# Performance work log

Measured on AMD Instinct MI355X. Metric: run time of the kernel, lower is better.

## Reference

```python
import jax, jax.numpy as jnp
import numpy as np

DIM = 25
N_NODES = 20000
N_EDGES = 320000
NFEAT = 300
NHID = 64
NCLASS = 50


def setup_inputs() -> dict:
    key = jax.random.key(0)
    ks = jax.random.split(key, 8)
    s1 = np.sqrt(6.0 / (NFEAT + NHID))
    s2 = np.sqrt(6.0 / (NHID * DIM + NCLASS))
    return {
        "x": jax.random.normal(ks[0], (N_NODES, NFEAT), dtype=jnp.float32),
        "adj_rows": jax.random.randint(ks[1], (DIM, N_EDGES), 0, N_NODES, dtype=jnp.int32),
        "adj_cols": jax.random.randint(ks[2], (DIM, N_EDGES), 0, N_NODES, dtype=jnp.int32),
        "adj_vals": jax.random.uniform(ks[3], (DIM, N_EDGES), dtype=jnp.float32),
        "W1": jax.random.uniform(ks[4], (DIM, NFEAT, NHID), dtype=jnp.float32, minval=-s1, maxval=s1),
        "b1": jnp.zeros((DIM, NHID), dtype=jnp.float32),
        "W2": jax.random.uniform(ks[5], (DIM, NHID * DIM, NCLASS), dtype=jnp.float32, minval=-s2, maxval=s2),
        "b2": jnp.zeros((DIM, NCLASS), dtype=jnp.float32),
    }


def _spmm(rows, cols, vals, sup, n):
    # sparse [n,n] @ dense [n,f] via gather + segment-sum scatter-add
    return jax.ops.segment_sum(vals[:, None] * sup[cols], rows, num_segments=n)


def reference(x, adj_rows, adj_cols, adj_vals, W1, b1, W2, b2):
    n = x.shape[0]
    spmm = jax.vmap(lambda r, c, v, s: _spmm(r, c, v, s, n))
    # layer 1: per-branch dense mm, spmm, bias, relu  -> [DIM, n, NHID]
    sup1 = jnp.einsum("nf,dfh->dnh", x, W1)
    h1 = jax.nn.relu(spmm(adj_rows, adj_cols, adj_vals, sup1) + b1[:, None, :])
    # permute + reshape: concat branch features per node -> [n, DIM*NHID]
    h1cat = jnp.transpose(h1, (1, 0, 2)).reshape(n, -1)
    # layer 2: per-branch dense mm, spmm, bias, relu -> [DIM, n, NCLASS]
    sup2 = jnp.einsum("nk,dkc->dnc", h1cat, W2)
    h2 = jax.nn.relu(spmm(adj_rows, adj_cols, adj_vals, sup2) + b2[:, None, :])
    # max-pool over branches (POOLING='max')
    return jnp.max(h2, axis=0)
```

## Files before the change

kernel.cpp:

```cpp
#include <hip/hip_runtime.h>
#include <hip/hip_bf16.h>
#include <cstdint>
#include <cstddef>

#define DIM 25
#define NN 20000
#define NE 320000
#define NF 300
#define NH 64
#define NC 50
#define K2 (DIM*NH)
#define KP1 320
#define B1T_ROWS 1664
#define B2T_ROWS 1280
#define NBK 79
#define EPB 4096
#define BPB ((NE + EPB - 1) / EPB)
#define FCAP 5632

typedef __attribute__((ext_vector_type(8))) short short8;
typedef __attribute__((ext_vector_type(4))) float floatx4;
typedef __hip_bfloat16 bf16;

static __device__ __forceinline__ unsigned bf16bits(float f) {
    bf16 b = __float2bfloat16(f);
    return (unsigned)*reinterpret_cast<unsigned short*>(&b);
}
static __device__ __forceinline__ float blo(unsigned w) { return __uint_as_float(w << 16); }
static __device__ __forceinline__ float bhi(unsigned w) { return __uint_as_float(w & 0xFFFF0000u); }

static __device__ __forceinline__ void gld16(const void* g, void* l) {
    __builtin_amdgcn_global_load_lds((const __attribute__((address_space(1))) unsigned*)g,
                                     (__attribute__((address_space(3))) unsigned*)l, 16, 0, 0);
}
static __device__ __forceinline__ unsigned lds_off(const void* p) {
    return (unsigned)(size_t)(const __attribute__((address_space(3))) char*)p;
}
#define DSR(dst, a, off) asm volatile("ds_read_b128 %0, %1 offset:" #off : "=v"(dst) : "v"(a))

__global__ void zero_kernel(int* __restrict__ p, int n) {
    int i = blockIdx.x * blockDim.x + threadIdx.x;
    if (i < n) p[i] = 0;
}

__global__ __launch_bounds__(256) void bucket_scatter_kernel(const int* __restrict__ rows,
                                                             const int* __restrict__ cols,
                                                             const float* __restrict__ vals,
                                                             int* __restrict__ gcur,
                                                             unsigned* __restrict__ interE,
                                                             unsigned char* __restrict__ interR) {
    const int d = blockIdx.y;
    const int e0 = blockIdx.x * EPB;
    __shared__ int lh[NBK];
    __shared__ int lo[NBK];
    __shared__ int lbase[NBK];
    __shared__ unsigned entE[EPB];
    __shared__ unsigned short entR[EPB];
    const int tid = threadIdx.x;
    for (int i = tid; i < NBK; i += 256) lh[i] = 0;
    __syncthreads();
    const int* rd = rows + (size_t)d * NE;
    const int* cd = cols + (size_t)d * NE;
    const float* vd = vals + (size_t)d * NE;
    const int e1 = min(e0 + EPB, NE);
    const int ne = e1 - e0;
    for (int i = e0 + tid; i < e1; i += 256)
        atomicAdd(&lh[rd[i] >> 8], 1);
    __syncthreads();
    if (tid == 0) {
        int run = 0;
        for (int b = 0; b < NBK; ++b) { lo[b] = run; run += lh[b]; }
    }
    __syncthreads();
    for (int i = tid; i < NBK; i += 256) {
        lbase[i] = lh[i] ? atomicAdd(&gcur[d * NBK + i], lh[i]) : 0;
        lh[i] = 0;
    }
    __syncthreads();
    for (int i = e0 + tid; i < e1; i += 256) {
        int r = rd[i];
        int b = r >> 8;
        int rank = atomicAdd(&lh[b], 1);
        int pos = lo[b] + rank;
        entE[pos] = (unsigned)cd[i] | (bf16bits(vd[i]) << 16);
        entR[pos] = (unsigned short)r;
    }
    __syncthreads();
    for (int p = tid; p < ne; p += 256) {
        int r = entR[p];
        int b = r >> 8;
        int gpos = lbase[b] + (p - lo[b]);
        if (gpos < FCAP) {
            size_t slot = ((size_t)d * NBK + b) * FCAP + gpos;
            interE[slot] = entE[p];
            interR[slot] = (unsigned char)r;
        }
    }
}

__global__ void bucket_scan_kernel(const int* __restrict__ gcur,
                                   int* __restrict__ offs_b,
                                   int* __restrict__ bcnt,
                                   int* __restrict__ offs) {
    const int d = blockIdx.x;
    if (threadIdx.x != 0) return;
    int run = 0;
    for (int b = 0; b < NBK; ++b) {
        int c = min(gcur[d * NBK + b], FCAP);
        offs_b[d * NBK + b] = run;
        bcnt[d * NBK + b] = c;
        run += c;
    }
    offs[d * (NN + 1) + NN] = run;
}

__global__ __launch_bounds__(256) void csr_finalize_kernel(const unsigned* __restrict__ interE,
                                                           const unsigned char* __restrict__ interR,
                                                           const int* __restrict__ offs_b,
                                                           const int* __restrict__ bcnt,
                                                           int* __restrict__ offs,
                                                           unsigned* __restrict__ sedge) {
    const int d = blockIdx.y;
    const int b = blockIdx.x;
    const int tid = threadIdx.x;
    const int s = offs_b[d * NBK + b];
    const int cnt = bcnt[d * NBK + b];
    const size_t base = ((size_t)d * NBK + b) * FCAP;
    __shared__ int sm[256];
    __shared__ int cur[256];
    __shared__ unsigned lse[FCAP];
    sm[tid] = 0;
    __syncthreads();
    for (int i = tid; i < cnt; i += 256)
        atomicAdd(&sm[interR[base + i]], 1);
    __syncthreads();
    int own = sm[tid];
    for (int off = 1; off < 256; off <<= 1) {
        int t = (tid >= off) ? sm[tid - off] : 0;
        __syncthreads();
        sm[tid] += t;
        __syncthreads();
    }
    int excl = sm[tid] - own;
    int row = (b << 8) + tid;
    if (row < NN) offs[d * (NN + 1) + row] = s + excl;
    cur[tid] = excl;
    __syncthreads();
    for (int i = tid; i < cnt; i += 256) {
        int idx = atomicAdd(&cur[interR[base + i]], 1);
        lse[idx] = interE[base + i];
    }
    __syncthreads();
    unsigned* sed = sedge + (size_t)d * NE;
    for (int t = tid; t < cnt; t += 256)
        sed[s + t] = lse[t];
}

__global__ void pack_x_kernel(const float* __restrict__ x, bf16* __restrict__ xb) {
    int i = blockIdx.x * blockDim.x + threadIdx.x;
    if (i >= NN * KP1) return;
    int n = i / KP1, k = i - n * KP1;
    xb[i] = __float2bfloat16((k < NF) ? x[(size_t)n * NF + k] : 0.f);
}

__global__ void pack_b1_kernel(const float* __restrict__ W1, bf16* __restrict__ b1t) {
    int i = blockIdx.x * blockDim.x + threadIdx.x;
    if (i >= B1T_ROWS * KP1) return;
    int j2 = i / KP1, k = i - j2 * KP1;
    int chunk = j2 >> 9;
    int r = j2 & 511;
    int d = chunk * 8 + (r >> 6);
    float v = 0.f;
    if (d < DIM && k < NF)
        v = W1[(size_t)d * NF * NH + (size_t)k * NH + (r & 63)];
    b1t[i] = __float2bfloat16(v);
}

__global__ void pack_b2_kernel(const float* __restrict__ W2, bf16* __restrict__ b2t) {
    int i = blockIdx.x * blockDim.x + threadIdx.x;
    if (i >= B2T_ROWS * K2) return;
    int r = i / K2, k = i - r * K2;
    float v = 0.f;
    if (r < DIM * NC) {
        int g = r / NC, c = r - g * NC;
        v = W2[(size_t)g * K2 * NC + (size_t)k * NC + c];
    }
    b2t[i] = __float2bfloat16(v);
}

__global__ __launch_bounds__(512, 2) void gemm256_bf16_kernel(const bf16* __restrict__ A, int lda,
                                                              const bf16* __restrict__ BT, int ldb,
                                                              bf16* __restrict__ C,
                                                              int ktiles, int mode, int nvalid) {
    __shared__ unsigned short As[2 * 256 * 64];
    __shared__ unsigned short Bs[2 * 256 * 64];
    const int tid = threadIdx.x;
    const int w = tid >> 6;
    const int l = tid & 63;
    const int MT = (int)gridDim.x;
    const int NT = (int)gridDim.y;
    const int bid = (int)blockIdx.y * MT + (int)blockIdx.x;
    const int pg = 8 * NT;
    const int grp = bid / pg;
    const int rem = bid - grp * pg;
    const int fm = grp * 8;
    const int gm = min(8, MT - fm);
    const int mt = fm + rem % gm;
    const int nt = rem / gm;
    const int m0 = mt * 256, n0 = nt * 256;
    const int wr = w >> 2, wc = w & 3;

    floatx4 acc[8][4] = {};

    const int strow = w * 8 + (l >> 3);
    const int gch = (l & 7) ^ (l >> 3);
    const bf16* pA[4];
    const bf16* pB[4];
    #pragma unroll
    for (int q = 0; q < 4; ++q) {
        pA[q] = A + (size_t)(m0 + q * 64 + strow) * lda + gch * 8;
        pB[q] = BT + (size_t)(n0 + q * 64 + strow) * ldb + gch * 8;
    }
    const unsigned slc0 = (unsigned)(((l >> 4)) ^ (l & 7)) * 16u;
    const unsigned slc1 = (unsigned)((4 + (l >> 4)) ^ (l & 7)) * 16u;
    const unsigned aRow = (unsigned)(wr * 128 + (l & 15)) * 128u;
    const unsigned bRow = (unsigned)(wc * 64 + (l & 15)) * 128u;
    const unsigned ldsA = lds_off(As), ldsB = lds_off(Bs);

    #pragma unroll
    for (int q = 0; q < 4; ++q) { gld16(pA[q], As + q * 4096 + w * 512); pA[q] += 64; }
    #pragma unroll
    for (int q = 0; q < 4; ++q) { gld16(pB[q], Bs + q * 4096 + w * 512); pB[q] += 64; }
    asm volatile("s_waitcnt vmcnt(0)");
    __builtin_amdgcn_sched_barrier(0);
    __builtin_amdgcn_s_barrier();
    __builtin_amdgcn_sched_barrier(0);

    short8 aF[4][2], bF[4][2];
    for (int kt = 0; kt < ktiles; ++kt) {
        const int c = kt & 1;
        const unsigned boff = (unsigned)c * 32768u;
        const unsigned aA0 = ldsA + boff + aRow + slc0;
        const unsigned aA1 = ldsA + boff + aRow + slc1;
        const unsigned bA0 = ldsB + boff + bRow + slc0;
        const unsigned bA1 = ldsB + boff + bRow + slc1;
        unsigned short* nA = As + (c ^ 1) * 16384 + w * 512;
        unsigned short* nB = Bs + (c ^ 1) * 16384 + w * 512;
        const bool stage = (kt + 1 < ktiles);
        DSR(aF[0][0], aA0, 0);    DSR(aF[0][1], aA1, 0);
        DSR(aF[1][0], aA0, 2048); DSR(aF[1][1], aA1, 2048);
        DSR(aF[2][0], aA0, 4096); DSR(aF[2][1], aA1, 4096);
        DSR(aF[3][0], aA0, 6144); DSR(aF[3][1], aA1, 6144);
        DSR(bF[0][0], bA0, 0);    DSR(bF[0][1], bA1, 0);
        DSR(bF[1][0], bA0, 2048); DSR(bF[1][1], bA1, 2048);
        if (stage) {
            gld16(pA[0], nA);         gld16(pA[1], nA + 4096);
            gld16(pA[2], nA + 8192);  gld16(pA[3], nA + 12288);
            pA[0] += 64; pA[1] += 64; pA[2] += 64; pA[3] += 64;
        }
        asm volatile("s_waitcnt lgkmcnt(0)");
        __builtin_amdgcn_sched_barrier(0);
        __builtin_amdgcn_s_setprio(1);
        #pragma unroll
        for (int mf = 0; mf < 4; ++mf)
            #pragma unroll
            for (int nf = 0; nf < 2; ++nf) {
                acc[mf][nf] = __builtin_amdgcn_mfma_f32_16x16x32_bf16(aF[mf][0], bF[nf][0], acc[mf][nf], 0, 0, 0);
                acc[mf][nf] = __builtin_amdgcn_mfma_f32_16x16x32_bf16(aF[mf][1], bF[nf][1], acc[mf][nf], 0, 0, 0);
            }
        __builtin_amdgcn_s_setprio(0);
        __builtin_amdgcn_sched_barrier(0);
        DSR(bF[2][0], bA0, 4096); DSR(bF[2][1], bA1, 4096);
        DSR(bF[3][0], bA0, 6144); DSR(bF[3][1], bA1, 6144);
        if (stage) {
            gld16(pB[0], nB);         gld16(pB[1], nB + 4096);
            gld16(pB[2], nB + 8192);  gld16(pB[3], nB + 12288);
            pB[0] += 64; pB[1] += 64; pB[2] += 64; pB[3] += 64;
        }
        asm volatile("s_waitcnt lgkmcnt(0)");
        __builtin_amdgcn_sched_barrier(0);
        __builtin_amdgcn_s_setprio(1);
        #pragma unroll
        for (int mf = 0; mf < 4; ++mf)
            #pragma unroll
            for (int nf = 2; nf < 4; ++nf) {
                acc[mf][nf] = __builtin_amdgcn_mfma_f32_16x16x32_bf16(aF[mf][0], bF[nf][0], acc[mf][nf], 0, 0, 0);
                acc[mf][nf] = __builtin_amdgcn_mfma_f32_16x16x32_bf16(aF[mf][1], bF[nf][1], acc[mf][nf], 0, 0, 0);
            }
        __builtin_amdgcn_s_setprio(0);
        __builtin_amdgcn_sched_barrier(0);
        DSR(aF[0][0], aA0, 8192);  DSR(aF[0][1], aA1, 8192);
        DSR(aF[1][0], aA0, 10240); DSR(aF[1][1], aA1, 10240);
        DSR(aF[2][0], aA0, 12288); DSR(aF[2][1], aA1, 12288);
        DSR(aF[3][0], aA0, 14336); DSR(aF[3][1], aA1, 14336);
        asm volatile("s_waitcnt lgkmcnt(0)");
        __builtin_amdgcn_sched_barrier(0);
        __builtin_amdgcn_s_setprio(1);
        #pragma unroll
        for (int mf = 0; mf < 4; ++mf)
            #pragma unroll
            for (int nf = 2; nf < 4; ++nf) {
                acc[mf + 4][nf] = __builtin_amdgcn_mfma_f32_16x16x32_bf16(aF[mf][0], bF[nf][0], acc[mf + 4][nf], 0, 0, 0);
                acc[mf + 4][nf] = __builtin_amdgcn_mfma_f32_16x16x32_bf16(aF[mf][1], bF[nf][1], acc[mf + 4][nf], 0, 0, 0);
            }
        __builtin_amdgcn_s_setprio(0);
        __builtin_amdgcn_sched_barrier(0);
        __builtin_amdgcn_s_setprio(1);
        #pragma unroll
        for (int mf = 0; mf < 4; ++mf)
            #pragma unroll
            for (int nf = 0; nf < 2; ++nf) {
                acc[mf + 4][nf] = __builtin_amdgcn_mfma_f32_16x16x32_bf16(aF[mf][0], bF[nf][0], acc[mf + 4][nf], 0, 0, 0);
                acc[mf + 4][nf] = __builtin_amdgcn_mfma_f32_16x16x32_bf16(aF[mf][1], bF[nf][1], acc[mf + 4][nf], 0, 0, 0);
            }
        __builtin_amdgcn_s_setprio(0);
        __builtin_amdgcn_sched_barrier(0);
        if (stage) {
            asm volatile("s_waitcnt vmcnt(0)");
            __builtin_amdgcn_sched_barrier(0);
            __builtin_amdgcn_s_barrier();
            __builtin_amdgcn_sched_barrier(0);
        }
    }
    const int cr = (l >> 4) * 4;
    const int cc = l & 15;
    #pragma unroll
    for (int mf = 0; mf < 8; ++mf) {
        #pragma unroll
        for (int r = 0; r < 4; ++r) {
            int m = m0 + wr * 128 + mf * 16 + cr + r;
            if (m >= NN) continue;
            #pragma unroll
            for (int nf = 0; nf < 4; ++nf) {
                int n = n0 + wc * 64 + nf * 16 + cc;
                if (n >= nvalid) continue;
                if (mode == 1) {
                    int g = n >> 6, h = n & 63;
                    C[(size_t)g * NN * NH + (size_t)m * NH + h] = __float2bfloat16(acc[mf][nf][r]);
                } else {
                    int g = n / NC, cl2 = n - g * NC;
                    C[(size_t)g * NN * NC + (size_t)m * NC + cl2] = __float2bfloat16(acc[mf][nf][r]);
                }
            }
        }
    }
}

__global__ __launch_bounds__(256) void gemm_bf16_kernel(const bf16* __restrict__ A, int lda,
                                                        const bf16* __restrict__ BT, int ldb,
                                                        bf16* __restrict__ C,
                                                        int ksteps, int mode, int nvalid) {
    __shared__ unsigned short As[3 * 128 * 32];
    __shared__ unsigned short Bs[3 * 128 * 32];
    const int tid = threadIdx.x;
    const int wave = tid >> 6;
    const int lane = tid & 63;
    const int mtiles = (int)gridDim.x;
    const int ntiles = (int)gridDim.y;
    const int bid = (int)blockIdx.y * mtiles + (int)blockIdx.x;
    const int per_group = 8 * ntiles;
    const int group = bid / per_group;
    const int rem = bid - group * per_group;
    const int first_m = group * 8;
    const int gm = min(8, mtiles - first_m);
    const int mt = first_m + rem % gm;
    const int nt = rem / gm;
    const int m0 = mt * 128;
    const int n0 = nt * 128;
    const int wm = (wave >> 1) * 64;
    const int wn = (wave & 1) * 64;
    floatx4 acc[4][4] = {};
    const int r0 = tid >> 2;
    const int cg = (tid & 3) ^ ((r0 >> 1) & 3);
    const int q8 = (lane >> 4) * 8;
    const int gq = q8 >> 3;
    unsigned short* lA0 = As + wave * 512;
    unsigned short* lA1 = As + 2048 + wave * 512;
    unsigned short* lB0 = Bs + wave * 512;
    unsigned short* lB1 = Bs + 2048 + wave * 512;
    const bf16* gA0 = A + (size_t)(m0 + r0) * lda + cg * 8;
    const bf16* gA1 = A + (size_t)(m0 + r0 + 64) * lda + cg * 8;
    const bf16* gB0 = BT + (size_t)(n0 + r0) * ldb + cg * 8;
    const bf16* gB1 = BT + (size_t)(n0 + r0 + 64) * ldb + cg * 8;
    int offA[4], offB[4];
    #pragma unroll
    for (int i = 0; i < 4; ++i) {
        int ra = wm + i * 16 + (lane & 15);
        int rb = wn + i * 16 + (lane & 15);
        offA[i] = ra * 32 + ((gq ^ ((ra >> 1) & 3)) << 3);
        offB[i] = rb * 32 + ((gq ^ ((rb >> 1) & 3)) << 3);
    }
    gld16(gA0, lA0); gld16(gA1, lA1); gld16(gB0, lB0); gld16(gB1, lB1);
    if (ksteps > 1) {
        gld16(gA0 + 32, lA0 + 4096); gld16(gA1 + 32, lA1 + 4096);
        gld16(gB0 + 32, lB0 + 4096); gld16(gB1 + 32, lB1 + 4096);
    }
    const bf16* pA0 = gA0 + 64;
    const bf16* pA1 = gA1 + 64;
    const bf16* pB0 = gB0 + 64;
    const bf16* pB1 = gB1 + 64;
    int buf = 0;
    int pbuf = 2;
    for (int ks = 0; ks < ksteps; ++ks) {
        if (ks + 1 < ksteps) asm volatile("s_waitcnt vmcnt(4)" ::: "memory");
        else                 asm volatile("s_waitcnt vmcnt(0)" ::: "memory");
        __builtin_amdgcn_sched_barrier(0);
        __builtin_amdgcn_s_barrier();
        __builtin_amdgcn_sched_barrier(0);
        if (ks + 2 < ksteps) {
            unsigned short* dA0 = lA0 + pbuf * 4096;
            unsigned short* dA1 = lA1 + pbuf * 4096;
            unsigned short* dB0 = lB0 + pbuf * 4096;
            unsigned short* dB1 = lB1 + pbuf * 4096;
            gld16(pA0, dA0); gld16(pA1, dA1); gld16(pB0, dB0); gld16(pB1, dB1);
            pA0 += 32; pA1 += 32; pB0 += 32; pB1 += 32;
            pbuf = (pbuf == 2) ? 0 : pbuf + 1;
        }
        const unsigned short* as = As + buf * 4096;
        const unsigned short* bs = Bs + buf * 4096;
        short8 af[4], bfr[4];
        #pragma unroll
        for (int i = 0; i < 4; ++i) {
            af[i]  = *(const short8*)&as[offA[i]];
            bfr[i] = *(const short8*)&bs[offB[i]];
        }
        #pragma unroll
        for (int i = 0; i < 4; ++i)
            #pragma unroll
            for (int j = 0; j < 4; ++j)
                acc[i][j] = __builtin_amdgcn_mfma_f32_16x16x32_bf16(af[i], bfr[j], acc[i][j], 0, 0, 0);
        buf = (buf == 2) ? 0 : buf + 1;
    }
    const int cr = (lane >> 4) * 4;
    const int cc = lane & 15;
    #pragma unroll
    for (int i = 0; i < 4; ++i) {
        #pragma unroll
        for (int r = 0; r < 4; ++r) {
            int m = m0 + wm + i * 16 + cr + r;
            if (m >= NN) continue;
            #pragma unroll
            for (int j = 0; j < 4; ++j) {
                int n = n0 + wn + j * 16 + cc;
                if (n >= nvalid) continue;
                if (mode == 1) {
                    int g = n >> 6, h = n & 63;
                    C[(size_t)g * NN * NH + (size_t)m * NH + h] = __float2bfloat16(acc[i][j][r]);
                } else {
                    int g = n / NC, c = n - g * NC;
                    C[(size_t)g * NN * NC + (size_t)m * NC + c] = __float2bfloat16(acc[i][j][r]);
                }
            }
        }
    }
}

__global__ __launch_bounds__(256) void spmm1_kernel(const bf16* __restrict__ sup,
                                                    const int* __restrict__ offs,
                                                    const unsigned* __restrict__ sedge,
                                                    const float* __restrict__ b1,
                                                    bf16* __restrict__ h1cat, int d0, int CHk) {
    const int i = blockIdx.x;
    const int g = i % CHk;
    const int nb = i / CHk;
    const int tid = threadIdx.x;
    const int lane = tid & 63;
    const int n = nb * 8 + ((tid >> 6) << 1) + (lane >> 5);
    const int hl = lane & 31;
    const int d = d0 + g;
    const int s = offs[d * (NN + 1) + n];
    const int e = offs[d * (NN + 1) + n + 1];
    const char* supd = (const char*)sup + (size_t)g * NN * NH * 2;
    const unsigned* sed = sedge + (size_t)d * NE;
    const unsigned hoff = (unsigned)hl * 4;
    float alo0 = 0.f, ahi0 = 0.f, alo1 = 0.f, ahi1 = 0.f;
    int j = s;
    for (; j + 4 <= e; j += 4) {
        unsigned e0 = sed[j], e1 = sed[j + 1], e2 = sed[j + 2], e3 = sed[j + 3];
        unsigned w0 = *(const unsigned*)(supd + (((e0 & 0xFFFFu) << 7) | hoff));
        unsigned w1 = *(const unsigned*)(supd + (((e1 & 0xFFFFu) << 7) | hoff));
        unsigned w2 = *(const unsigned*)(supd + (((e2 & 0xFFFFu) << 7) | hoff));
        unsigned w3 = *(const unsigned*)(supd + (((e3 & 0xFFFFu) << 7) | hoff));
        float v0 = bhi(e0), v1 = bhi(e1), v2 = bhi(e2), v3 = bhi(e3);
        alo0 = fmaf(v0, blo(w0), alo0); ahi0 = fmaf(v0, bhi(w0), ahi0);
        alo1 = fmaf(v1, blo(w1), alo1); ahi1 = fmaf(v1, bhi(w1), ahi1);
        alo0 = fmaf(v2, blo(w2), alo0); ahi0 = fmaf(v2, bhi(w2), ahi0);
        alo1 = fmaf(v3, blo(w3), alo1); ahi1 = fmaf(v3, bhi(w3), ahi1);
    }
    for (; j < e; ++j) {
        unsigned e0 = sed[j];
        unsigned w0 = *(const unsigned*)(supd + (((e0 & 0xFFFFu) << 7) | hoff));
        float v0 = bhi(e0);
        alo0 = fmaf(v0, blo(w0), alo0); ahi0 = fmaf(v0, bhi(w0), ahi0);
    }
    float alo = fmaxf((alo0 + alo1) + b1[d * NH + 2 * hl], 0.f);
    float ahi = fmaxf((ahi0 + ahi1) + b1[d * NH + 2 * hl + 1], 0.f);
    unsigned packed = bf16bits(alo) | (bf16bits(ahi) << 16);
    *(unsigned*)((char*)h1cat + ((size_t)n * K2 + d * NH) * 2 + hoff) = packed;
}

__global__ __launch_bounds__(256) void spmm2b_kernel(const bf16* __restrict__ sup2,
                                                     const int* __restrict__ offs,
                                                     const unsigned* __restrict__ sedge,
                                                     const float* __restrict__ b2,
                                                     unsigned* __restrict__ h2u) {
    const int i = blockIdx.x;
    const int r = i & 7;
    const int q = i >> 3;
    int d, nb;
    if (q < 7500) { d = r + 8 * (q / 2500); nb = q % 2500; }
    else { d = 24; nb = (q - 7500) * 8 + r; if (nb >= 2500) return; }
    const int tid = threadIdx.x;
    const int lane = tid & 63;
    const int n = nb * 8 + ((tid >> 6) << 1) + (lane >> 5);
    const int cl = min(lane & 31, 24);
    const unsigned coff = (unsigned)cl * 4;
    const int s = offs[d * (NN + 1) + n];
    const int e = offs[d * (NN + 1) + n + 1];
    const char* supd = (const char*)sup2 + (size_t)d * NN * NC * 2;
    const unsigned* sed = sedge + (size_t)d * NE;
    float alo0 = b2[d * NC + 2 * cl], ahi0 = b2[d * NC + 2 * cl + 1];
    float alo1 = 0.f, ahi1 = 0.f;
    int j = s;
    for (; j + 4 <= e; j += 4) {
        unsigned e0 = sed[j], e1 = sed[j + 1], e2 = sed[j + 2], e3 = sed[j + 3];
        unsigned w0 = *(const unsigned*)(supd + ((e0 & 0xFFFFu) * 100u + coff));
        unsigned w1 = *(const unsigned*)(supd + ((e1 & 0xFFFFu) * 100u + coff));
        unsigned w2 = *(const unsigned*)(supd + ((e2 & 0xFFFFu) * 100u + coff));
        unsigned w3 = *(const unsigned*)(supd + ((e3 & 0xFFFFu) * 100u + coff));
        float v0 = bhi(e0), v1 = bhi(e1), v2 = bhi(e2), v3 = bhi(e3);
        alo0 = fmaf(v0, blo(w0), alo0); ahi0 = fmaf(v0, bhi(w0), ahi0);
        alo1 = fmaf(v1, blo(w1), alo1); ahi1 = fmaf(v1, bhi(w1), ahi1);
        alo0 = fmaf(v2, blo(w2), alo0); ahi0 = fmaf(v2, bhi(w2), ahi0);
        alo1 = fmaf(v3, blo(w3), alo1); ahi1 = fmaf(v3, bhi(w3), ahi1);
    }
    for (; j < e; ++j) {
        unsigned e0 = sed[j];
        unsigned w0 = *(const unsigned*)(supd + ((e0 & 0xFFFFu) * 100u + coff));
        float v0 = bhi(e0);
        alo0 = fmaf(v0, blo(w0), alo0); ahi0 = fmaf(v0, bhi(w0), ahi0);
    }
    float alo = fmaxf(alo0 + alo1, 0.f);
    float ahi = fmaxf(ahi0 + ahi1, 0.f);
    if ((lane & 31) < 25)
        h2u[((size_t)d * NN + n) * 25 + cl] = bf16bits(alo) | (bf16bits(ahi) << 16);
}

__global__ __launch_bounds__(256) void maxk_kernel(const unsigned* __restrict__ h2u,
                                                   float* __restrict__ out) {
    int i = blockIdx.x * blockDim.x + threadIdx.x;
    if (i >= NN * 25) return;
    int n = i / 25, cl = i - n * 25;
    float mlo = 0.f, mhi = 0.f;
    #pragma unroll
    for (int d = 0; d < DIM; ++d) {
        unsigned w = h2u[(size_t)d * NN * 25 + i];
        mlo = fmaxf(mlo, blo(w));
        mhi = fmaxf(mhi, bhi(w));
    }
    *(float2*)&out[(size_t)n * NC + 2 * cl] = make_float2(mlo, mhi);
}

extern "C" void kernel_launch(void* const* d_in, const int* in_sizes, int n_in,
                              void* d_out, int out_size, void* d_ws, size_t ws_size,
                              hipStream_t stream) {
    const float* x    = (const float*)d_in[0];
    const int*   rows = (const int*)d_in[1];
    const int*   cols = (const int*)d_in[2];
    const float* vals = (const float*)d_in[3];
    const float* W1   = (const float*)d_in[4];
    const float* b1   = (const float*)d_in[5];
    const float* W2   = (const float*)d_in[6];
    const float* b2   = (const float*)d_in[7];
    float* out = (float*)d_out;

    char* ws = (char*)d_ws;
    size_t off = 0;
    auto alloc = [&](size_t bytes) {
        void* p = ws + off;
        off += (bytes + 255) & ~(size_t)255;
        return p;
    };
    bf16* supbuf = (bf16*)alloc(sizeof(bf16) * (size_t)DIM * NN * NC);
    bf16* h1cat  = (bf16*)alloc(sizeof(bf16) * (size_t)NN * K2);
    bf16* b1t    = (bf16*)alloc(sizeof(bf16) * (size_t)B1T_ROWS * KP1);
    bf16* b2t    = (bf16*)alloc(sizeof(bf16) * (size_t)B2T_ROWS * K2);
    int*  offs   = (int*)alloc(sizeof(int) * (size_t)DIM * (NN + 1));
    int*  gcur   = (int*)alloc(sizeof(int) * (size_t)DIM * NBK);
    int*  offs_b = (int*)alloc(sizeof(int) * (size_t)DIM * NBK);
    int*  bcnt   = (int*)alloc(sizeof(int) * (size_t)DIM * NBK);
    unsigned* sedge = (unsigned*)alloc(sizeof(unsigned) * (size_t)DIM * NE);

    bf16* sup1 = supbuf;
    bf16* xbf  = supbuf + (size_t)12 * 1024 * 1024;
    bf16* sup2 = supbuf;
    unsigned* interE = (unsigned*)h1cat;
    unsigned char* interR = (unsigned char*)h1cat + (size_t)DIM * NBK * FCAP * 4;
    unsigned* h2u = (unsigned*)h1cat;

    if (off > ws_size) return;

    zero_kernel<<<(DIM * NBK + 255) / 256, 256, 0, stream>>>(gcur, DIM * NBK);
    bucket_scatter_kernel<<<dim3(BPB, DIM), 256, 0, stream>>>(rows, cols, vals, gcur, interE, interR);
    bucket_scan_kernel<<<DIM, 64, 0, stream>>>(gcur, offs_b, bcnt, offs);
    csr_finalize_kernel<<<dim3(NBK, DIM), 256, 0, stream>>>(interE, interR, offs_b, bcnt, offs, sedge);

    pack_x_kernel<<<(NN * KP1 + 255) / 256, 256, 0, stream>>>(x, xbf);
    pack_b1_kernel<<<(B1T_ROWS * KP1 + 255) / 256, 256, 0, stream>>>(W1, b1t);
    pack_b2_kernel<<<(B2T_ROWS * K2 + 255) / 256, 256, 0, stream>>>(W2, b2t);

    const int mtiles128 = (NN + 127) / 128;
    const int mtiles256 = (NN + 255) / 256;

    const int cstart[4] = {0, 8, 16, 24};
    const int csize[4]  = {8, 8, 8, 1};
    const int crow[4]   = {0, 512, 1024, 1536};
    for (int c = 0; c < 3; ++c) {
        gemm256_bf16_kernel<<<dim3(mtiles256, 2), 512, 0, stream>>>(
            xbf, KP1, b1t + (size_t)crow[c] * KP1, KP1, sup1, KP1 / 64, 1, 512);
        spmm1_kernel<<<csize[c] * (NN / 8), 256, 0, stream>>>(
            sup1, offs, sedge, b1, h1cat, cstart[c], csize[c]);
    }
    gemm_bf16_kernel<<<dim3(mtiles128, 1), 256, 0, stream>>>(
        xbf, KP1, b1t + (size_t)crow[3] * KP1, KP1, sup1, KP1 / 32, 1, 64);
    spmm1_kernel<<<csize[3] * (NN / 8), 256, 0, stream>>>(
        sup1, offs, sedge, b1, h1cat, cstart[3], csize[3]);

    gemm256_bf16_kernel<<<dim3(mtiles256, B2T_ROWS / 256), 512, 0, stream>>>(
        h1cat, K2, b2t, K2, sup2, K2 / 64, 2, DIM * NC);
    spmm2b_kernel<<<8 * 7813, 256, 0, stream>>>(sup2, offs, sedge, b2, h2u);
    maxk_kernel<<<(NN * 25 + 255) / 256, 256, 0, stream>>>(h2u, out);
}
```

Measured before the change: 727.8 us.

## Split each node's edge list across two half-waves and software-pipeline gathers

Both SpMM kernels now assign one wavefront per destination node instead of two nodes per wave. The two 32-lane halves process alternating edges and combine their partial sums with a cross-half shuffle. The 4-way unrolled loop is replaced by a software-pipelined loop that prefetches the next edge index and feature word. This roughly halves the serial chain per lane and adds latency hiding, at the cost of doubling the block count and using half-idle lanes in the final store.

```diff
diff --git a/kernel.cpp b/kernel.cpp
--- a/kernel.cpp
+++ b/kernel.cpp
@@ -465,38 +465,47 @@
     const int nb = i / CHk;
     const int tid = threadIdx.x;
     const int lane = tid & 63;
-    const int n = nb * 8 + ((tid >> 6) << 1) + (lane >> 5);
+    const int n = nb * 4 + (tid >> 6);
+    const int eh = lane >> 5;
     const int hl = lane & 31;
     const int d = d0 + g;
     const int s = offs[d * (NN + 1) + n];
     const int e = offs[d * (NN + 1) + n + 1];
     const char* supd = (const char*)sup + (size_t)g * NN * NH * 2;
-    const unsigned* sed = sedge + (size_t)d * NE;
+    const unsigned* p = sedge + (size_t)d * NE + s + eh;
     const unsigned hoff = (unsigned)hl * 4;
-    float alo0 = 0.f, ahi0 = 0.f, alo1 = 0.f, ahi1 = 0.f;
-    int j = s;
-    for (; j + 4 <= e; j += 4) {
-        unsigned e0 = sed[j], e1 = sed[j + 1], e2 = sed[j + 2], e3 = sed[j + 3];
-        unsigned w0 = *(const unsigned*)(supd + (((e0 & 0xFFFFu) << 7) | hoff));
-        unsigned w1 = *(const unsigned*)(supd + (((e1 & 0xFFFFu) << 7) | hoff));
-        unsigned w2 = *(const unsigned*)(supd + (((e2 & 0xFFFFu) << 7) | hoff));
-        unsigned w3 = *(const unsigned*)(supd + (((e3 & 0xFFFFu) << 7) | hoff));
-        float v0 = bhi(e0), v1 = bhi(e1), v2 = bhi(e2), v3 = bhi(e3);
-        alo0 = fmaf(v0, blo(w0), alo0); ahi0 = fmaf(v0, bhi(w0), ahi0);
-        alo1 = fmaf(v1, blo(w1), alo1); ahi1 = fmaf(v1, bhi(w1), ahi1);
-        alo0 = fmaf(v2, blo(w2), alo0); ahi0 = fmaf(v2, bhi(w2), ahi0);
-        alo1 = fmaf(v3, blo(w3), alo1); ahi1 = fmaf(v3, bhi(w3), ahi1);
-    }
-    for (; j < e; ++j) {
-        unsigned e0 = sed[j];
-        unsigned w0 = *(const unsigned*)(supd + (((e0 & 0xFFFFu) << 7) | hoff));
-        float v0 = bhi(e0);
-        alo0 = fmaf(v0, blo(w0), alo0); ahi0 = fmaf(v0, bhi(w0), ahi0);
-    }
-    float alo = fmaxf((alo0 + alo1) + b1[d * NH + 2 * hl], 0.f);
-    float ahi = fmaxf((ahi0 + ahi1) + b1[d * NH + 2 * hl + 1], 0.f);
-    unsigned packed = bf16bits(alo) | (bf16bits(ahi) << 16);
-    *(unsigned*)((char*)h1cat + ((size_t)n * K2 + d * NH) * 2 + hoff) = packed;
+    float alo = 0.f, ahi = 0.f;
+    const int rem = e - s - eh;
+    const int cnt = (rem > 0) ? ((rem + 1) >> 1) : 0;
+    unsigned ea = 0, eb = 0, wv = 0;
+    if (cnt >= 1) ea = p[0];
+    if (cnt >= 2) eb = p[2];
+    if (cnt >= 1) wv = *(const unsigned*)(supd + (((ea & 0xFFFFu) << 7) | hoff));
+    for (int k = 0; k + 2 < cnt; ++k) {
+        unsigned ec = p[2 * k + 4];
+        unsigned wn = *(const unsigned*)(supd + (((eb & 0xFFFFu) << 7) | hoff));
+        float v = bhi(ea);
+        alo = fmaf(v, blo(wv), alo); ahi = fmaf(v, bhi(wv), ahi);
+        ea = eb; wv = wn; eb = ec;
+    }
+    if (cnt >= 2) {
+        unsigned wn = *(const unsigned*)(supd + (((eb & 0xFFFFu) << 7) | hoff));
+        float v = bhi(ea);
+        alo = fmaf(v, blo(wv), alo); ahi = fmaf(v, bhi(wv), ahi);
+        ea = eb; wv = wn;
+    }
+    if (cnt >= 1) {
+        float v = bhi(ea);
+        alo = fmaf(v, blo(wv), alo); ahi = fmaf(v, bhi(wv), ahi);
+    }
+    alo += __shfl_xor(alo, 32, 64);
+    ahi += __shfl_xor(ahi, 32, 64);
+    if (lane < 32) {
+        float flo = fmaxf(alo + b1[d * NH + 2 * hl], 0.f);
+        float fhi = fmaxf(ahi + b1[d * NH + 2 * hl + 1], 0.f);
+        unsigned packed = bf16bits(flo) | (bf16bits(fhi) << 16);
+        *(unsigned*)((char*)h1cat + ((size_t)n * K2 + d * NH) * 2 + hoff) = packed;
+    }
 }
 
 __global__ __launch_bounds__(256) void spmm2b_kernel(const bf16* __restrict__ sup2,
@@ -508,42 +517,49 @@
     const int r = i & 7;
     const int q = i >> 3;
     int d, nb;
-    if (q < 7500) { d = r + 8 * (q / 2500); nb = q % 2500; }
-    else { d = 24; nb = (q - 7500) * 8 + r; if (nb >= 2500) return; }
+    if (q < 15000) { d = r + 8 * (q / 5000); nb = q % 5000; }
+    else { d = 24; nb = (q - 15000) * 8 + r; if (nb >= 5000) return; }
     const int tid = threadIdx.x;
     const int lane = tid & 63;
-    const int n = nb * 8 + ((tid >> 6) << 1) + (lane >> 5);
+    const int n = nb * 4 + (tid >> 6);
+    const int eh = lane >> 5;
     const int cl = min(lane & 31, 24);
     const unsigned coff = (unsigned)cl * 4;
     const int s = offs[d * (NN + 1) + n];
     const int e = offs[d * (NN + 1) + n + 1];
     const char* supd = (const char*)sup2 + (size_t)d * NN * NC * 2;
-    const unsigned* sed = sedge + (size_t)d * NE;
-    float alo0 = b2[d * NC + 2 * cl], ahi0 = b2[d * NC + 2 * cl + 1];
-    float alo1 = 0.f, ahi1 = 0.f;
-    int j = s;
-    for (; j + 4 <= e; j += 4) {
-        unsigned e0 = sed[j], e1 = sed[j + 1], e2 = sed[j + 2], e3 = sed[j + 3];
-        unsigned w0 = *(const unsigned*)(supd + ((e0 & 0xFFFFu) * 100u + coff));
-        unsigned w1 = *(const unsigned*)(supd + ((e1 & 0xFFFFu) * 100u + coff));
-        unsigned w2 = *(const unsigned*)(supd + ((e2 & 0xFFFFu) * 100u + coff));
-        unsigned w3 = *(const unsigned*)(supd + ((e3 & 0xFFFFu) * 100u + coff));
-        float v0 = bhi(e0), v1 = bhi(e1), v2 = bhi(e2), v3 = bhi(e3);
-        alo0 = fmaf(v0, blo(w0), alo0); ahi0 = fmaf(v0, bhi(w0), ahi0);
-        alo1 = fmaf(v1, blo(w1), alo1); ahi1 = fmaf(v1, bhi(w1), ahi1);
-        alo0 = fmaf(v2, blo(w2), alo0); ahi0 = fmaf(v2, bhi(w2), ahi0);
-        alo1 = fmaf(v3, blo(w3), alo1); ahi1 = fmaf(v3, bhi(w3), ahi1);
-    }
-    for (; j < e; ++j) {
-        unsigned e0 = sed[j];
-        unsigned w0 = *(const unsigned*)(supd + ((e0 & 0xFFFFu) * 100u + coff));
-        float v0 = bhi(e0);
-        alo0 = fmaf(v0, blo(w0), alo0); ahi0 = fmaf(v0, bhi(w0), ahi0);
-    }
-    float alo = fmaxf(alo0 + alo1, 0.f);
-    float ahi = fmaxf(ahi0 + ahi1, 0.f);
-    if ((lane & 31) < 25)
-        h2u[((size_t)d * NN + n) * 25 + cl] = bf16bits(alo) | (bf16bits(ahi) << 16);
+    const unsigned* p = sedge + (size_t)d * NE + s + eh;
+    float alo = 0.f, ahi = 0.f;
+    const int rem = e - s - eh;
+    const int cnt = (rem > 0) ? ((rem + 1) >> 1) : 0;
+    unsigned ea = 0, eb = 0, wv = 0;
+    if (cnt >= 1) ea = p[0];
+    if (cnt >= 2) eb = p[2];
+    if (cnt >= 1) wv = *(const unsigned*)(supd + ((ea & 0xFFFFu) * 100u + coff));
+    for (int k = 0; k + 2 < cnt; ++k) {
+        unsigned ec = p[2 * k + 4];
+        unsigned wn = *(const unsigned*)(supd + ((eb & 0xFFFFu) * 100u + coff));
+        float v = bhi(ea);
+        alo = fmaf(v, blo(wv), alo); ahi = fmaf(v, bhi(wv), ahi);
+        ea = eb; wv = wn; eb = ec;
+    }
+    if (cnt >= 2) {
+        unsigned wn = *(const unsigned*)(supd + ((eb & 0xFFFFu) * 100u + coff));
+        float v = bhi(ea);
+        alo = fmaf(v, blo(wv), alo); ahi = fmaf(v, bhi(wv), ahi);
+        ea = eb; wv = wn;
+    }
+    if (cnt >= 1) {
+        float v = bhi(ea);
+        alo = fmaf(v, blo(wv), alo); ahi = fmaf(v, bhi(wv), ahi);
+    }
+    alo += __shfl_xor(alo, 32, 64);
+    ahi += __shfl_xor(ahi, 32, 64);
+    if (lane < 25) {
+        float flo = fmaxf(alo + b2[d * NC + 2 * cl], 0.f);
+        float fhi = fmaxf(ahi + b2[d * NC + 2 * cl + 1], 0.f);
+        h2u[((size_t)d * NN + n) * 25 + cl] = bf16bits(flo) | (bf16bits(fhi) << 16);
+    }
 }
 
 __global__ __launch_bounds__(256) void maxk_kernel(const unsigned* __restrict__ h2u,
@@ -618,16 +634,16 @@
     for (int c = 0; c < 3; ++c) {
         gemm256_bf16_kernel<<<dim3(mtiles256, 2), 512, 0, stream>>>(
             xbf, KP1, b1t + (size_t)crow[c] * KP1, KP1, sup1, KP1 / 64, 1, 512);
-        spmm1_kernel<<<csize[c] * (NN / 8), 256, 0, stream>>>(
+        spmm1_kernel<<<csize[c] * (NN / 4), 256, 0, stream>>>(
             sup1, offs, sedge, b1, h1cat, cstart[c], csize[c]);
     }
     gemm_bf16_kernel<<<dim3(mtiles128, 1), 256, 0, stream>>>(
         xbf, KP1, b1t + (size_t)crow[3] * KP1, KP1, sup1, KP1 / 32, 1, 64);
-    spmm1_kernel<<<csize[3] * (NN / 8), 256, 0, stream>>>(
+    spmm1_kernel<<<csize[3] * (NN / 4), 256, 0, stream>>>(
         sup1, offs, sedge, b1, h1cat, cstart[3], csize[3]);
 
     gemm256_bf16_kernel<<<dim3(mtiles256, B2T_ROWS / 256), 512, 0, stream>>>(
         h1cat, K2, b2t, K2, sup2, K2 / 64, 2, DIM * NC);
-    spmm2b_kernel<<<8 * 7813, 256, 0, stream>>>(sup2, offs, sedge, b2, h2u);
+    spmm2b_kernel<<<8 * 15625, 256, 0, stream>>>(sup2, offs, sedge, b2, h2u);
     maxk_kernel<<<(NN * 25 + 255) / 256, 256, 0, stream>>>(h2u, out);
 }
```

Measured after the change: 853.1 us. 1.17x slower.
